# Kernel optimization log

Hardware: AMD Instinct MI355X
Metric: run time of the kernel (lower is better)

The kernel has to match this reference:

```python
import jax, jax.numpy as jnp
import numpy as np

N_NODES = 100000
N_EDGES = 1600000
IN_DIM, HID_DIM, OUT_DIM = 128, 128, 64


def setup_inputs() -> dict:
    key = jax.random.key(0)
    k1, k2, k3, k4 = jax.random.split(key, 4)
    x = jax.random.normal(k1, (N_NODES, IN_DIM), dtype=jnp.float32)
    edge_index = jax.random.randint(k2, (2, N_EDGES), 0, N_NODES, dtype=jnp.int64)
    # Glorot-ish init for weights, zeros for biases (as in PyG GCNConv defaults)
    W1 = jax.random.normal(k3, (IN_DIM, HID_DIM), dtype=jnp.float32) * (1.0 / np.sqrt(IN_DIM))
    b1 = jnp.zeros((HID_DIM,), dtype=jnp.float32)
    W2 = jax.random.normal(k4, (HID_DIM, OUT_DIM), dtype=jnp.float32) * (1.0 / np.sqrt(HID_DIM))
    b2 = jnp.zeros((OUT_DIM,), dtype=jnp.float32)
    return {"x": x, "edge_index": edge_index, "W1": W1, "b1": b1, "W2": W2, "b2": b2}


def _build_norm(edge_index, num_nodes):
    """Add self-loops and compute symmetric GCN normalization per edge.
    Returns (src, dst, norm) with self-loops appended."""
    loops = jnp.arange(num_nodes, dtype=edge_index.dtype)
    src = jnp.concatenate([edge_index[0], loops])
    dst = jnpp_concat = jnp.concatenate([edge_index[1], loops])
    deg = jax.ops.segment_sum(jnp.ones_like(dst, dtype=jnp.float32), dst,
                              num_segments=num_nodes)
    dinv = jax.lax.rsqrt(deg)  # deg >= 1 due to self-loops
    norm = dinv[src] * dinv[dst]  # [E + N]
    return src, dst, norm


def _gcn_conv(h, W, b, src, dst, norm, num_nodes):
    h = h @ W                                   # [N, F_out]
    msg = h[src] * norm[:, None]                # gather + scale, [E+N, F_out]
    agg = jax.ops.segment_sum(msg, dst, num_segments=num_nodes)
    return agg + b


def reference(x, edge_index, W1, b1, W2, b2):
    num_nodes = x.shape[0]
    src, dst, norm = _build_norm(edge_index, num_nodes)
    h = jax.nn.relu(_gcn_conv(x, W1, b1, src, dst, norm, num_nodes))
    return _gcn_conv(h, W2, b2, src, dst, norm, num_nodes)
```

## Files before the change

kernel.cpp:

```cpp
#include <hip/hip_runtime.h>

#define NN 100000
#define NE 1600000
#define NB 782
#define NBPAD 1024
#define CAPB 3072
#define EPB 8192
#define NROWPAD 100096
#define DPAD 136
#define OPAD 72

typedef __attribute__((ext_vector_type(8))) short short8;
typedef __attribute__((ext_vector_type(4))) float f32x4;

__device__ __forceinline__ unsigned short bf16rn(float f) {
    unsigned u = __float_as_uint(f);
    return (unsigned short)((u + 0x7FFFu + ((u >> 16) & 1u)) >> 16);
}
__device__ __forceinline__ uint2 packbf4(float4 v) {
    uint2 u;
    u.x = (unsigned)bf16rn(v.x) | ((unsigned)bf16rn(v.y) << 16);
    u.y = (unsigned)bf16rn(v.z) | ((unsigned)bf16rn(v.w) << 16);
    return u;
}
__device__ __forceinline__ unsigned packbf2(float x, float y) {
    return (unsigned)bf16rn(x) | ((unsigned)bf16rn(y) << 16);
}
__device__ __forceinline__ void bf8acc(float* a, uint4 v, float q) {
    a[0] = fmaf(__uint_as_float(v.x << 16), q, a[0]);
    a[1] = fmaf(__uint_as_float(v.x & 0xFFFF0000u), q, a[1]);
    a[2] = fmaf(__uint_as_float(v.y << 16), q, a[2]);
    a[3] = fmaf(__uint_as_float(v.y & 0xFFFF0000u), q, a[3]);
    a[4] = fmaf(__uint_as_float(v.z << 16), q, a[4]);
    a[5] = fmaf(__uint_as_float(v.z & 0xFFFF0000u), q, a[5]);
    a[6] = fmaf(__uint_as_float(v.w << 16), q, a[6]);
    a[7] = fmaf(__uint_as_float(v.w & 0xFFFF0000u), q, a[7]);
}
__device__ __forceinline__ uint2 ldnt2(const unsigned long long* p) {
    unsigned long long v = __builtin_nontemporal_load(p);
    uint2 r;
    r.x = (unsigned)v;
    r.y = (unsigned)(v >> 32);
    return r;
}

__global__ void detect_i64_k(const unsigned* __restrict__ ei, int* __restrict__ flag) {
    unsigned w = ei[2 * threadIdx.x + 1];
    unsigned long long b = __ballot(w == 0u);
    if (threadIdx.x == 0) *flag = (b == 0xFFFFFFFFFFFFFFFFull) ? 1 : 0;
}
__device__ __forceinline__ int load_node(const void* ei, int i64, long long idx) {
    return i64 ? (int)((const long long*)ei)[idx] : ((const int*)ei)[idx];
}

__global__ void cast_bf16_k(const float* __restrict__ in, ushort* __restrict__ outb,
                            long long n4) {
    long long i = (long long)blockIdx.x * 256 + threadIdx.x;
    if (i >= n4) return;
    ((uint2*)outb)[i] = packbf4(((const float4*)in)[i]);
}

__global__ void prep_wt_k(const float* __restrict__ W1, const float* __restrict__ W2,
                          ushort* __restrict__ W1t, ushort* __restrict__ W2t) {
    int i = blockIdx.x * 256 + threadIdx.x;
    if (i < 128 * 128) {
        int k = i >> 7, n = i & 127;
        W1t[n * 128 + k] = bf16rn(W1[k * 128 + n]);
    }
    if (i < 128 * 64) {
        int k = i >> 6, n = i & 63;
        W2t[n * 128 + k] = bf16rn(W2[k * 64 + n]);
    }
}

__global__ __launch_bounds__(256) void binfill_k(const void* __restrict__ ei,
                                                 const int* __restrict__ flag,
                                                 int* __restrict__ cur,
                                                 unsigned* __restrict__ bstage) {
    __shared__ unsigned binned[EPB];
    __shared__ int lcnt[NBPAD];
    __shared__ int lpos[NBPAD];
    __shared__ int gbase[NBPAD];
    __shared__ int tsum[256];
    int tid = threadIdx.x;
    long long e0 = (long long)blockIdx.x * EPB;
    int i64 = *flag;

    for (int i = tid; i < NBPAD; i += 256) lcnt[i] = 0;
    __syncthreads();

    for (int i = tid; i < EPB; i += 256) {
        long long e = e0 + i;
        if (e < NE) {
            int d = load_node(ei, i64, (long long)NE + e);
            atomicAdd(&lcnt[d >> 7], 1);
        }
    }
    __syncthreads();

    int base = tid * 4;
    int c0 = lcnt[base], c1 = lcnt[base + 1], c2 = lcnt[base + 2], c3 = lcnt[base + 3];
    int s = c0 + c1 + c2 + c3;
    tsum[tid] = s;
    __syncthreads();
    for (int off = 1; off < 256; off <<= 1) {
        int v = (tid >= off) ? tsum[tid - off] : 0;
        __syncthreads();
        tsum[tid] += v;
        __syncthreads();
    }
    int excl = tsum[tid] - s;
    int p0 = excl, p1 = excl + c0, p2 = p1 + c1, p3 = p2 + c2;
    lcnt[base] = p0; lcnt[base + 1] = p1; lcnt[base + 2] = p2; lcnt[base + 3] = p3;
    lpos[base] = p0; lpos[base + 1] = p1; lpos[base + 2] = p2; lpos[base + 3] = p3;
    if (base < NB)     gbase[base]     = c0 ? atomicAdd(&cur[base], c0) : 0;
    if (base + 1 < NB) gbase[base + 1] = c1 ? atomicAdd(&cur[base + 1], c1) : 0;
    if (base + 2 < NB) gbase[base + 2] = c2 ? atomicAdd(&cur[base + 2], c2) : 0;
    if (base + 3 < NB) gbase[base + 3] = c3 ? atomicAdd(&cur[base + 3], c3) : 0;
    __syncthreads();

    for (int i = tid; i < EPB; i += 256) {
        long long e = e0 + i;
        if (e < NE) {
            int sv = load_node(ei, i64, e);
            int d  = load_node(ei, i64, (long long)NE + e);
            int b  = d >> 7;
            int p  = atomicAdd(&lpos[b], 1);
            binned[p] = ((unsigned)(d & 127) << 17) | (unsigned)sv;
        }
    }
    __syncthreads();

    for (int b = tid; b < NB; b += 256) {
        int start = lcnt[b], endp = lpos[b];
        int gb = gbase[b];
        unsigned* dst = bstage + (long long)b * CAPB;
        for (int k = start; k < endp; k++) {
            int go = gb + (k - start);
            if (go < CAPB) dst[go] = binned[k];
        }
    }
}

__global__ __launch_bounds__(256) void regroup_k(const int* __restrict__ cur,
                                                 const unsigned* __restrict__ bstage,
                                                 int* __restrict__ cnt,
                                                 int* __restrict__ rowstart,
                                                 uint2* __restrict__ g2,
                                                 float* __restrict__ dinv) {
    __shared__ unsigned stash[CAPB];
    __shared__ int lcnt[128], lofs[128], lpos[128], sc[128];
    int tid = threadIdx.x;
    int b = blockIdx.x;

    int total = cur[b];
    if (total > CAPB) total = CAPB;
    const unsigned* seg = bstage + (long long)b * CAPB;
    for (int i = tid; i < total; i += 256) stash[i] = seg[i];
    __syncthreads();

    if (tid < 128) { lcnt[tid] = 0; lpos[tid] = 0; }
    __syncthreads();
    for (int i = tid; i < total; i += 256)
        atomicAdd(&lcnt[stash[i] >> 17], 1);
    __syncthreads();

    if (tid < 128) sc[tid] = lcnt[tid];
    __syncthreads();
    for (int off = 1; off < 128; off <<= 1) {
        int v = 0;
        if (tid < 128 && tid >= off) v = sc[tid - off];
        __syncthreads();
        if (tid < 128) sc[tid] += v;
        __syncthreads();
    }
    if (tid < 128) {
        lofs[tid] = sc[tid] - lcnt[tid];
        int node = b * 128 + tid;
        if (node < NN) {
            cnt[node] = lcnt[tid];
            rowstart[node] = b * CAPB + lofs[tid];
            dinv[node] = rsqrtf((float)(lcnt[tid] + 1));
        }
    }
    __syncthreads();

    uint2* g = g2 + (long long)b * CAPB;
    for (int i = tid; i < total; i += 256) {
        unsigned e = stash[i];
        int nl = e >> 17;
        int p = atomicAdd(&lpos[nl], 1);
        g[lofs[nl] + p] = make_uint2(e & 0x1FFFFu, (unsigned)(b * 128 + nl));
    }
}

__global__ __launch_bounds__(256) void qn_k(const int* __restrict__ cur,
                                            const float* __restrict__ dinv,
                                            uint2* __restrict__ g2) {
    int b = blockIdx.x;
    int total = cur[b];
    if (total > CAPB) total = CAPB;
    uint2* g = g2 + (long long)b * CAPB;
    for (int i = threadIdx.x; i < total; i += 256) {
        uint2 e = g[i];
        float q = dinv[e.x] * dinv[e.y];
        g[i] = make_uint2(e.x, __float_as_uint(q));
    }
}

template <int LPN>
__device__ __forceinline__ void gf4(const uint4* __restrict__ h4, int lane,
                                    uint2 e0, uint2 e1, uint2 e2, uint2 e3,
                                    float* a, float* b) {
    uint4 v0 = h4[e0.x * LPN + lane];
    uint4 v1 = h4[e1.x * LPN + lane];
    uint4 v2 = h4[e2.x * LPN + lane];
    uint4 v3 = h4[e3.x * LPN + lane];
    bf8acc(a, v0, __uint_as_float(e0.y));
    bf8acc(b, v1, __uint_as_float(e1.y));
    bf8acc(a, v2, __uint_as_float(e2.y));
    bf8acc(b, v3, __uint_as_float(e3.y));
}

template <int LPN, bool BIAS, bool OUTB>
__global__ __launch_bounds__(256) void pull2_k(const uint2* __restrict__ g2,
                                               const int* __restrict__ rowstart,
                                               const int* __restrict__ cnt,
                                               const float* __restrict__ dinv,
                                               const ushort* __restrict__ hb,
                                               const float* __restrict__ bias,
                                               void* __restrict__ out) {
    int tid = threadIdx.x;
    int node = blockIdx.x * (256 / LPN) + tid / LPN;
    int lane = tid & (LPN - 1);
    if (node >= NN) return;

    const uint4* h4 = (const uint4*)hb;
    float di = dinv[node];
    float w0 = di * di;
    float a[8] = {0.f, 0.f, 0.f, 0.f, 0.f, 0.f, 0.f, 0.f};
    float b[8] = {0.f, 0.f, 0.f, 0.f, 0.f, 0.f, 0.f, 0.f};
    bf8acc(a, h4[(unsigned)node * LPN + lane], w0);

    int deg = cnt[node];
    const unsigned long long* rowq =
        (const unsigned long long*)(g2 + rowstart[node]);

    int j = 0;
    if (deg >= 8) {
        uint2 e0 = ldnt2(rowq + 0), e1 = ldnt2(rowq + 1);
        uint2 e2 = ldnt2(rowq + 2), e3 = ldnt2(rowq + 3);
        for (; j + 7 < deg; j += 4) {
            uint2 f0 = ldnt2(rowq + j + 4), f1 = ldnt2(rowq + j + 5);
            uint2 f2 = ldnt2(rowq + j + 6), f3 = ldnt2(rowq + j + 7);
            gf4<LPN>(h4, lane, e0, e1, e2, e3, a, b);
            e0 = f0; e1 = f1; e2 = f2; e3 = f3;
        }
        gf4<LPN>(h4, lane, e0, e1, e2, e3, a, b);
        j += 4;
    } else if (deg >= 4) {
        gf4<LPN>(h4, lane, ldnt2(rowq + 0), ldnt2(rowq + 1),
                 ldnt2(rowq + 2), ldnt2(rowq + 3), a, b);
        j = 4;
    }
    for (; j < deg; j++) {
        uint2 e = ldnt2(rowq + j);
        bf8acc(a, h4[e.x * LPN + lane], __uint_as_float(e.y));
    }

    float o[8];
#pragma unroll
    for (int k = 0; k < 8; k++) o[k] = a[k] + b[k];
    if (BIAS) {
        float4 b0 = ((const float4*)bias)[2 * lane];
        float4 b1 = ((const float4*)bias)[2 * lane + 1];
        o[0] += b0.x; o[1] += b0.y; o[2] += b0.z; o[3] += b0.w;
        o[4] += b1.x; o[5] += b1.y; o[6] += b1.z; o[7] += b1.w;
    }
    if (OUTB) {
        uint4 p;
        p.x = packbf2(o[0], o[1]);
        p.y = packbf2(o[2], o[3]);
        p.z = packbf2(o[4], o[5]);
        p.w = packbf2(o[6], o[7]);
        ((uint4*)out)[(unsigned)node * LPN + lane] = p;
    } else {
        float4 lo = make_float4(o[0], o[1], o[2], o[3]);
        float4 hi = make_float4(o[4], o[5], o[6], o[7]);
        ((float4*)out)[(unsigned)node * (2 * LPN) + 2 * lane] = lo;
        ((float4*)out)[(unsigned)node * (2 * LPN) + 2 * lane + 1] = hi;
    }
}

__global__ __launch_bounds__(256) void dgemm_mfma_k(const ushort* __restrict__ Ab,
                                                    const ushort* __restrict__ W1t,
                                                    const float* __restrict__ b1,
                                                    const ushort* __restrict__ W2t,
                                                    ushort* __restrict__ H2b) {
    __shared__ ushort Tt[4][32 * DPAD];
    __shared__ ushort Ot[4][32 * OPAD];
    int tid = threadIdx.x;
    int wv = tid >> 6, lane = tid & 63;
    int m16 = lane & 15, quad = lane >> 4;
    int row0 = blockIdx.x * 128 + wv * 32;

    short8 af[2][4];
#pragma unroll
    for (int mt = 0; mt < 2; mt++)
#pragma unroll
        for (int kc = 0; kc < 4; kc++)
            af[mt][kc] = *(const short8*)(Ab + (long long)(row0 + mt * 16 + m16) * 128
                                          + kc * 32 + quad * 8);
    f32x4 accA[2][8];
#pragma unroll
    for (int mt = 0; mt < 2; mt++)
#pragma unroll
        for (int nt = 0; nt < 8; nt++) accA[mt][nt] = (f32x4){0.f, 0.f, 0.f, 0.f};

#pragma unroll
    for (int nt = 0; nt < 8; nt++) {
#pragma unroll
        for (int kc = 0; kc < 4; kc++) {
            short8 bf = *(const short8*)(W1t + (nt * 16 + m16) * 128 + kc * 32 + quad * 8);
            accA[0][nt] = __builtin_amdgcn_mfma_f32_16x16x32_bf16(af[0][kc], bf, accA[0][nt], 0, 0, 0);
            accA[1][nt] = __builtin_amdgcn_mfma_f32_16x16x32_bf16(af[1][kc], bf, accA[1][nt], 0, 0, 0);
        }
    }

#pragma unroll
    for (int nt = 0; nt < 8; nt++) {
        float bb = b1[nt * 16 + m16];
#pragma unroll
        for (int mt = 0; mt < 2; mt++)
#pragma unroll
            for (int r = 0; r < 4; r++) {
                float v = fmaxf(accA[mt][nt][r] + bb, 0.f);
                Tt[wv][(mt * 16 + quad * 4 + r) * DPAD + nt * 16 + m16] = bf16rn(v);
            }
    }
    __syncthreads();

    f32x4 accB[2][4];
#pragma unroll
    for (int mt = 0; mt < 2; mt++)
#pragma unroll
        for (int nt = 0; nt < 4; nt++) accB[mt][nt] = (f32x4){0.f, 0.f, 0.f, 0.f};

#pragma unroll
    for (int nt = 0; nt < 4; nt++) {
#pragma unroll
        for (int kc = 0; kc < 4; kc++) {
            short8 bf = *(const short8*)(W2t + (nt * 16 + m16) * 128 + kc * 32 + quad * 8);
#pragma unroll
            for (int mt = 0; mt < 2; mt++) {
                short8 aT = *(const short8*)(&Tt[wv][(mt * 16 + m16) * DPAD + kc * 32 + quad * 8]);
                accB[mt][nt] = __builtin_amdgcn_mfma_f32_16x16x32_bf16(aT, bf, accB[mt][nt], 0, 0, 0);
            }
        }
    }

#pragma unroll
    for (int nt = 0; nt < 4; nt++)
#pragma unroll
        for (int mt = 0; mt < 2; mt++)
#pragma unroll
            for (int r = 0; r < 4; r++)
                Ot[wv][(mt * 16 + quad * 4 + r) * OPAD + nt * 16 + m16] = bf16rn(accB[mt][nt][r]);
    __syncthreads();

    uint4* H4 = (uint4*)H2b;
#pragma unroll
    for (int it = 0; it < 4; it++) {
        int idx = it * 64 + lane;
        int r = idx >> 3, c = idx & 7;
        int grow = row0 + r;
        if (grow < NN) {
            uint4 v = *(const uint4*)(&Ot[wv][r * OPAD + c * 8]);
            H4[(long long)grow * 8 + c] = v;
        }
    }
}

extern "C" void kernel_launch(void* const* d_in, const int* in_sizes, int n_in,
                              void* d_out, int out_size, void* d_ws, size_t ws_size,
                              hipStream_t stream) {
    const float* x  = (const float*)d_in[0];
    const void*  ei = d_in[1];
    const float* W1 = (const float*)d_in[2];
    const float* b1 = (const float*)d_in[3];
    const float* W2 = (const float*)d_in[4];
    const float* b2 = (const float*)d_in[5];
    float* out = (float*)d_out;
    char* ws = (char*)d_ws;

    int*      flag     = (int*)ws;
    int*      cur      = (int*)(ws + 0x1000);
    int*      cnt      = (int*)(ws + 0x10000);
    int*      rowstart = (int*)(ws + 0x80000);
    unsigned* bstage   = (unsigned*)(ws + 0x100000);
    uint2*    g2       = (uint2*)(ws + 0xB00000);
    ushort*   xb       = (ushort*)(ws + 0x1E00000);
    ushort*   aggxb    = (ushort*)(ws + 0x3700000);
    ushort*   h2b      = (ushort*)(ws + 0x5000000);
    ushort*   W1t      = (ushort*)(ws + 0x5D00000);
    ushort*   W2t      = (ushort*)(ws + 0x5D10000);
    float*    dinv     = (float*)(ws + 0x5D20000);

    hipMemsetAsync(cur, 0, NB * sizeof(int), stream);
    detect_i64_k<<<1, 64, 0, stream>>>((const unsigned*)ei, flag);
    cast_bf16_k<<<(NN * 32 + 255) / 256, 256, 0, stream>>>(x, xb, (long long)NN * 32);
    prep_wt_k<<<64, 256, 0, stream>>>(W1, W2, W1t, W2t);
    binfill_k<<<(NE + EPB - 1) / EPB, 256, 0, stream>>>(ei, flag, cur, bstage);
    regroup_k<<<NB, 256, 0, stream>>>(cur, bstage, cnt, rowstart, g2, dinv);
    qn_k<<<NB, 256, 0, stream>>>(cur, dinv, g2);

    pull2_k<16, false, true><<<(NN + 15) / 16, 256, 0, stream>>>(g2, rowstart, cnt, dinv,
                                                                 xb, nullptr, aggxb);
    dgemm_mfma_k<<<NROWPAD / 128, 256, 0, stream>>>(aggxb, W1t, b1, W2t, h2b);

    pull2_k<8, true, false><<<(NN + 31) / 32, 256, 0, stream>>>(g2, rowstart, cnt, dinv,
                                                                h2b, b2, out);
}
```

Measured before the change: 335.0 us.

## Narrow per-lane gather to 4 features and software-pipeline neighbor row loads

The pull aggregation kernel now gives each lane 4 bf16 features (8-byte loads) instead of 8 (16-byte loads), doubling lanes per node to 32 for layer 1 and 16 for layer 2. The main loop is restructured to prefetch the next four edges and their feature gathers before accumulating the current ones. Non-temporal edge loads are replaced with plain loads. This aims to raise parallelism and keep more gathers in flight, at the cost of more threads each re-reading the edge list and doing narrower memory transactions.

```diff
diff --git a/kernel.cpp b/kernel.cpp
--- a/kernel.cpp
+++ b/kernel.cpp
@@ -17,31 +17,26 @@
     unsigned u = __float_as_uint(f);
     return (unsigned short)((u + 0x7FFFu + ((u >> 16) & 1u)) >> 16);
 }
+__device__ __forceinline__ float4 bf2x4(uint2 g) {
+    float4 r;
+    r.x = __uint_as_float(g.x << 16);
+    r.y = __uint_as_float(g.x & 0xFFFF0000u);
+    r.z = __uint_as_float(g.y << 16);
+    r.w = __uint_as_float(g.y & 0xFFFF0000u);
+    return r;
+}
 __device__ __forceinline__ uint2 packbf4(float4 v) {
     uint2 u;
     u.x = (unsigned)bf16rn(v.x) | ((unsigned)bf16rn(v.y) << 16);
     u.y = (unsigned)bf16rn(v.z) | ((unsigned)bf16rn(v.w) << 16);
     return u;
 }
-__device__ __forceinline__ unsigned packbf2(float x, float y) {
-    return (unsigned)bf16rn(x) | ((unsigned)bf16rn(y) << 16);
-}
-__device__ __forceinline__ void bf8acc(float* a, uint4 v, float q) {
-    a[0] = fmaf(__uint_as_float(v.x << 16), q, a[0]);
-    a[1] = fmaf(__uint_as_float(v.x & 0xFFFF0000u), q, a[1]);
-    a[2] = fmaf(__uint_as_float(v.y << 16), q, a[2]);
-    a[3] = fmaf(__uint_as_float(v.y & 0xFFFF0000u), q, a[3]);
-    a[4] = fmaf(__uint_as_float(v.z << 16), q, a[4]);
-    a[5] = fmaf(__uint_as_float(v.z & 0xFFFF0000u), q, a[5]);
-    a[6] = fmaf(__uint_as_float(v.w << 16), q, a[6]);
-    a[7] = fmaf(__uint_as_float(v.w & 0xFFFF0000u), q, a[7]);
-}
-__device__ __forceinline__ uint2 ldnt2(const unsigned long long* p) {
-    unsigned long long v = __builtin_nontemporal_load(p);
-    uint2 r;
-    r.x = (unsigned)v;
-    r.y = (unsigned)(v >> 32);
-    return r;
+__device__ __forceinline__ void acc4(float4& a, uint2 v, unsigned qb) {
+    float q = __uint_as_float(qb);
+    a.x = fmaf(__uint_as_float(v.x << 16), q, a.x);
+    a.y = fmaf(__uint_as_float(v.x & 0xFFFF0000u), q, a.y);
+    a.z = fmaf(__uint_as_float(v.y << 16), q, a.z);
+    a.w = fmaf(__uint_as_float(v.y & 0xFFFF0000u), q, a.w);
 }
 
 __global__ void detect_i64_k(const unsigned* __restrict__ ei, int* __restrict__ flag) {
@@ -208,22 +203,8 @@
     }
 }
 
-template <int LPN>
-__device__ __forceinline__ void gf4(const uint4* __restrict__ h4, int lane,
-                                    uint2 e0, uint2 e1, uint2 e2, uint2 e3,
-                                    float* a, float* b) {
-    uint4 v0 = h4[e0.x * LPN + lane];
-    uint4 v1 = h4[e1.x * LPN + lane];
-    uint4 v2 = h4[e2.x * LPN + lane];
-    uint4 v3 = h4[e3.x * LPN + lane];
-    bf8acc(a, v0, __uint_as_float(e0.y));
-    bf8acc(b, v1, __uint_as_float(e1.y));
-    bf8acc(a, v2, __uint_as_float(e2.y));
-    bf8acc(b, v3, __uint_as_float(e3.y));
-}
-
 template <int LPN, bool BIAS, bool OUTB>
-__global__ __launch_bounds__(256) void pull2_k(const uint2* __restrict__ g2,
+__global__ __launch_bounds__(256) void pull3_k(const uint2* __restrict__ g2,
                                                const int* __restrict__ rowstart,
                                                const int* __restrict__ cnt,
                                                const float* __restrict__ dinv,
@@ -235,61 +216,57 @@
     int lane = tid & (LPN - 1);
     if (node >= NN) return;
 
-    const uint4* h4 = (const uint4*)hb;
+    const uint2* h2 = (const uint2*)hb;
     float di = dinv[node];
     float w0 = di * di;
-    float a[8] = {0.f, 0.f, 0.f, 0.f, 0.f, 0.f, 0.f, 0.f};
-    float b[8] = {0.f, 0.f, 0.f, 0.f, 0.f, 0.f, 0.f, 0.f};
-    bf8acc(a, h4[(unsigned)node * LPN + lane], w0);
+    float4 A = make_float4(0.f, 0.f, 0.f, 0.f);
+    float4 B = make_float4(0.f, 0.f, 0.f, 0.f);
+    {
+        float4 hv = bf2x4(h2[(unsigned)node * LPN + lane]);
+        A.x = hv.x * w0; A.y = hv.y * w0; A.z = hv.z * w0; A.w = hv.w * w0;
+    }
 
     int deg = cnt[node];
-    const unsigned long long* rowq =
-        (const unsigned long long*)(g2 + rowstart[node]);
+    const uint2* row = g2 + rowstart[node];
 
     int j = 0;
-    if (deg >= 8) {
-        uint2 e0 = ldnt2(rowq + 0), e1 = ldnt2(rowq + 1);
-        uint2 e2 = ldnt2(rowq + 2), e3 = ldnt2(rowq + 3);
-        for (; j + 7 < deg; j += 4) {
-            uint2 f0 = ldnt2(rowq + j + 4), f1 = ldnt2(rowq + j + 5);
-            uint2 f2 = ldnt2(rowq + j + 6), f3 = ldnt2(rowq + j + 7);
-            gf4<LPN>(h4, lane, e0, e1, e2, e3, a, b);
+    if (deg >= 4) {
+        uint2 e0 = row[0], e1 = row[1], e2 = row[2], e3 = row[3];
+        uint2 v0 = h2[e0.x * LPN + lane];
+        uint2 v1 = h2[e1.x * LPN + lane];
+        uint2 v2 = h2[e2.x * LPN + lane];
+        uint2 v3 = h2[e3.x * LPN + lane];
+        for (; j + 8 <= deg; j += 4) {
+            uint2 f0 = row[j + 4], f1 = row[j + 5], f2 = row[j + 6], f3 = row[j + 7];
+            acc4(A, v0, e0.y); acc4(B, v1, e1.y);
+            acc4(A, v2, e2.y); acc4(B, v3, e3.y);
+            uint2 w0v = h2[f0.x * LPN + lane];
+            uint2 w1v = h2[f1.x * LPN + lane];
+            uint2 w2v = h2[f2.x * LPN + lane];
+            uint2 w3v = h2[f3.x * LPN + lane];
             e0 = f0; e1 = f1; e2 = f2; e3 = f3;
-        }
-        gf4<LPN>(h4, lane, e0, e1, e2, e3, a, b);
+            v0 = w0v; v1 = w1v; v2 = w2v; v3 = w3v;
+        }
+        acc4(A, v0, e0.y); acc4(B, v1, e1.y);
+        acc4(A, v2, e2.y); acc4(B, v3, e3.y);
         j += 4;
-    } else if (deg >= 4) {
-        gf4<LPN>(h4, lane, ldnt2(rowq + 0), ldnt2(rowq + 1),
-                 ldnt2(rowq + 2), ldnt2(rowq + 3), a, b);
-        j = 4;
     }
     for (; j < deg; j++) {
-        uint2 e = ldnt2(rowq + j);
-        bf8acc(a, h4[e.x * LPN + lane], __uint_as_float(e.y));
-    }
-
-    float o[8];
-#pragma unroll
-    for (int k = 0; k < 8; k++) o[k] = a[k] + b[k];
+        uint2 e = row[j];
+        uint2 v = h2[e.x * LPN + lane];
+        acc4(A, v, e.y);
+    }
+
+    float4 o;
+    o.x = A.x + B.x; o.y = A.y + B.y; o.z = A.z + B.z; o.w = A.w + B.w;
     if (BIAS) {
-        float4 b0 = ((const float4*)bias)[2 * lane];
-        float4 b1 = ((const float4*)bias)[2 * lane + 1];
-        o[0] += b0.x; o[1] += b0.y; o[2] += b0.z; o[3] += b0.w;
-        o[4] += b1.x; o[5] += b1.y; o[6] += b1.z; o[7] += b1.w;
-    }
-    if (OUTB) {
-        uint4 p;
-        p.x = packbf2(o[0], o[1]);
-        p.y = packbf2(o[2], o[3]);
-        p.z = packbf2(o[4], o[5]);
-        p.w = packbf2(o[6], o[7]);
-        ((uint4*)out)[(unsigned)node * LPN + lane] = p;
-    } else {
-        float4 lo = make_float4(o[0], o[1], o[2], o[3]);
-        float4 hi = make_float4(o[4], o[5], o[6], o[7]);
-        ((float4*)out)[(unsigned)node * (2 * LPN) + 2 * lane] = lo;
-        ((float4*)out)[(unsigned)node * (2 * LPN) + 2 * lane + 1] = hi;
-    }
+        float4 bb = ((const float4*)bias)[lane];
+        o.x += bb.x; o.y += bb.y; o.z += bb.z; o.w += bb.w;
+    }
+    if (OUTB)
+        ((uint2*)out)[(unsigned)node * LPN + lane] = packbf4(o);
+    else
+        ((float4*)out)[(unsigned)node * LPN + lane] = o;
 }
 
 __global__ __launch_bounds__(256) void dgemm_mfma_k(const ushort* __restrict__ Ab,
@@ -414,10 +391,10 @@
     regroup_k<<<NB, 256, 0, stream>>>(cur, bstage, cnt, rowstart, g2, dinv);
     qn_k<<<NB, 256, 0, stream>>>(cur, dinv, g2);
 
-    pull2_k<16, false, true><<<(NN + 15) / 16, 256, 0, stream>>>(g2, rowstart, cnt, dinv,
-                                                                 xb, nullptr, aggxb);
+    pull3_k<32, false, true><<<(NN + 7) / 8, 256, 0, stream>>>(g2, rowstart, cnt, dinv,
+                                                               xb, nullptr, aggxb);
     dgemm_mfma_k<<<NROWPAD / 128, 256, 0, stream>>>(aggxb, W1t, b1, W2t, h2b);
 
-    pull2_k<8, true, false><<<(NN + 31) / 32, 256, 0, stream>>>(g2, rowstart, cnt, dinv,
-                                                                h2b, b2, out);
-}
+    pull3_k<16, true, false><<<(NN + 15) / 16, 256, 0, stream>>>(g2, rowstart, cnt, dinv,
+                                                                 h2b, b2, out);
+}
```

Measured after the change: 325.7 us. 2.8% less time.
